# Optimization experiments

Measured on AMD Instinct MI355X. Metric: run time of the kernel, lower is better.

## Reference

```python
import jax, jax.numpy as jnp
import numpy as np

B, N, K = 8, 2048, 100  # graphs per batch, nodes per graph, diffpool clusters


def _bn(x, g, b, eps=1e-5):
    # BatchNorm1d in training mode over all B*N nodes (biased variance)
    m = x.mean(axis=(0, 1))
    v = x.var(axis=(0, 1))
    return (x - m) * jax.lax.rsqrt(v + eps) * g + b


def _norm_adj(A):
    # PyG gcn_norm: add remaining self-loops (fill=1), D^-1/2 (A+I) D^-1/2
    n = A.shape[-1]
    d = jnp.diagonal(A, axis1=-2, axis2=-1)
    A_hat = A + jnp.where(d == 0, 1.0, 0.0)[..., :, None] * jnp.eye(n, dtype=A.dtype)
    deg = A_hat.sum(-1)
    dinv = jnp.where(deg > 0, 1.0 / jnp.sqrt(deg), 0.0)
    return dinv[..., :, None] * A_hat * dinv[..., None, :]


def _gcn(An, x, W, b):
    # GCNConv: propagate(x @ W) + bias, with pre-normalized adjacency
    return An @ (x @ W) + b


def _forward(x, adj, W_in, W3030, Wp13, b30, b100, Wfc_pool, bfc_pool,
             W1, b1, W2, b2, gamma30, beta30, gamma100, beta100):
    A_w = _norm_adj(adj)                               # weighted (edge_attr) adjacency
    A_b = _norm_adj((adj > 0).astype(adj.dtype))       # pool convs ignore edge_attr
    # feature branch
    x11 = _bn(_gcn(A_w, x, W_in[0], b30[0]), gamma30[0], beta30[0])
    x12 = _bn(_gcn(A_w, x11, W3030[0], b30[1]), gamma30[1], beta30[1])
    x13 = _bn(_gcn(A_w, x12, W3030[1], b30[2]), gamma30[2], beta30[2])
    x1_out = jnp.concatenate([x11, x12, x13], -1).max(axis=1)   # [B,90]
    # assignment branch
    s11 = _bn(_gcn(A_b, x, W_in[1], b30[3]), gamma30[3], beta30[3])
    s12 = _bn(_gcn(A_b, s11, W3030[2], b30[4]), gamma30[4], beta30[4])
    s13 = _bn(_gcn(A_b, s12, Wp13, b100), gamma100, beta100)
    s1 = jnp.concatenate([s11, s12, s13], -1) @ Wfc_pool + bfc_pool  # [B,N,K]
    # dense_diff_pool (link/entropy losses are unused by the forward output)
    s = jax.nn.softmax(s1, -1)
    p1_x = jnp.einsum('bnk,bnd->bkd', s, x13)          # s^T x  [B,K,30]
    p1_adj = jnp.einsum('bnk,bnl->bkl', s, adj @ s)    # s^T A s  [B,K,K]
    # second stage on pooled (dense, weighted) graph
    A2 = _norm_adj(p1_adj)
    x21 = _bn(_gcn(A2, p1_x, W3030[3], b30[5]), gamma30[5], beta30[5])
    x22 = _bn(_gcn(A2, x21, W3030[4], b30[6]), gamma30[6], beta30[6])
    x23 = _bn(_gcn(A2, x22, W3030[5], b30[7]), gamma30[7], beta30[7])
    x2_out = jnp.concatenate([x21, x22, x23], -1).max(axis=1)   # [B,90]
    h = jnp.concatenate([x1_out, x2_out], -1) @ W1 + b1
    return jax.nn.relu(h) @ W2 + b2                    # [B,6]


def setup_inputs():
    key = jax.random.key(0)
    ks = jax.random.split(key, 12)
    u = jax.random.uniform(ks[0], (B, N, N), dtype=jnp.float32)
    mask = jax.random.uniform(ks[1], (B, N, N)) < 0.05
    A = jnp.triu(u * mask, 1)
    adj = A + jnp.swapaxes(A, -1, -2)
    x = jax.random.normal(ks[2], (B, N, 3), dtype=jnp.float32)
    w = lambda k, s: jax.random.normal(k, s, dtype=jnp.float32) * 0.1
    return dict(
        x=x, adj=adj,
        W_in=w(ks[3], (2, 3, 30)),      # conv11, pool_conv11
        W3030=w(ks[4], (6, 30, 30)),    # conv12, conv13, pool_conv12, conv21..23
        Wp13=w(ks[5], (30, 100)),
        b30=jnp.zeros((8, 30), jnp.float32),
        b100=jnp.zeros((100,), jnp.float32),
        Wfc_pool=w(ks[6], (160, 100)), bfc_pool=jnp.zeros((100,), jnp.float32),
        W1=w(ks[7], (180, 50)), b1=jnp.zeros((50,), jnp.float32),
        W2=w(ks[8], (50, 6)), b2=jnp.zeros((6,), jnp.float32),
        gamma30=jnp.ones((8, 30), jnp.float32), beta30=jnp.zeros((8, 30), jnp.float32),
        gamma100=jnp.ones((100,), jnp.float32), beta100=jnp.zeros((100,), jnp.float32),
    )


def reference(x, adj, W_in, W3030, Wp13, b30, b100, Wfc_pool, bfc_pool,
              W1, b1, W2, b2, gamma30, beta30, gamma100, beta100):
    return _forward(x, adj, W_in, W3030, Wp13, b30, b100, Wfc_pool, bfc_pool,
                    W1, b1, W2, b2, gamma30, beta30, gamma100, beta100)
```

## Files before the change

kernel.cpp:

```cpp
#include <hip/hip_runtime.h>
#include <hip/hip_fp16.h>
#include <cstdint>
#include <cstddef>

#define BATCH 8
#define NN 2048
#define RTOT 16384

static constexpr size_t OF_B1W   = 0;
static constexpr size_t OF_B1B   = 3840;
static constexpr size_t OF_B2W   = 7680;
static constexpr size_t OF_B2B   = 11520;
static constexpr size_t OF_B3W   = 15360;
static constexpr size_t OF_B3B   = 15840;
static constexpr size_t OF_S2    = 17440;
static constexpr size_t OF_CNT   = 17620;
static constexpr size_t ZEND     = 17632;
static constexpr size_t OF_DINVW = 17664;
static constexpr size_t OF_DINVB = OF_DINVW + 16384;
static constexpr size_t OF_HWBT  = OF_DINVB + 16384;
static constexpr size_t OF_HW3T  = OF_HWBT + 524288;
static constexpr size_t OF_HBT   = OF_HW3T + 262144;
static constexpr size_t OF_ZW    = OF_HBT + 917504;
static constexpr size_t OF_ZB    = OF_ZW + 524288;
static constexpr size_t OF_X11   = OF_ZB + 1703936;
static constexpr size_t OF_X12   = OF_X11 + 524288;
static constexpr size_t OF_X13   = OF_X12 + 524288;
static constexpr size_t OF_S11   = OF_X13 + 524288;
static constexpr size_t OF_S12   = OF_S11 + 524288;
static constexpr size_t OF_PARTMAX = OF_S12 + 524288;
static constexpr size_t OF_PP    = OF_PARTMAX + 23040;
static constexpr size_t OF_PPOOL = OF_PP + 3328000;
static constexpr size_t OF_AW    = OF_PPOOL + 104000;
static constexpr size_t OF_AB    = OF_AW + 16777216;
static constexpr size_t OF_SROW  = OF_AB + 16777216;

typedef _Float16 f16x8 __attribute__((ext_vector_type(8)));
typedef float f32x4 __attribute__((ext_vector_type(4)));

#define FMA4(acc, s, h) { acc.x += (s)*(h).x; acc.y += (s)*(h).y; acc.z += (s)*(h).z; acc.w += (s)*(h).w; }

__device__ __forceinline__ unsigned short f2h(float f) {
  _Float16 h = (_Float16)f;
  return *(unsigned short*)&h;
}
__device__ __forceinline__ float h2f(unsigned short s) {
  _Float16 h = *(_Float16*)&s;
  return (float)h;
}

__device__ __forceinline__ size_t fidx(size_t blk, int lc, int k) {
  return ((blk * 64 + (k >> 5)) * 64 + ((k >> 3) & 3) * 16 + lc) * 8 + (k & 7);
}


__global__ __launch_bounds__(256) void k_build(
    const float* __restrict__ adj, const float* __restrict__ x,
    const float* __restrict__ Win,
    _Float16* __restrict__ Aw, _Float16* __restrict__ Ab,
    float* __restrict__ dinvw, float* __restrict__ dinvb,
    _Float16* __restrict__ HT, float* __restrict__ zbase)
{
  __shared__ float tile[16*516];
  __shared__ float dshw[16], dshb[16];
  int t = threadIdx.x;
  int blk = blockIdx.x;
  int r0 = blk << 4;
  size_t gph = (size_t)(r0 >> 11);
  if (blk < 69) {
    int zi = blk * 256 + t;
    if (zi < (int)ZEND) zbase[zi] = 0.f;
  }
  int lr = t >> 4, ls = t & 15;
  const float* rowp = adj + (size_t)(r0 + lr) * NN;
  float sum = 0.f; int cnt = 0;
  for (int ch = 0; ch < 4; ++ch) {
    int c0 = ch << 9;
    __syncthreads();
    const float4* rp = (const float4*)(rowp + c0);
#pragma unroll
    for (int i = 0; i < 8; ++i) {
      float4 v = rp[ls + (i << 4)];
      sum += v.x + v.y + v.z + v.w;
      cnt += (v.x != 0.f) + (v.y != 0.f) + (v.z != 0.f) + (v.w != 0.f);
      *(float4*)&tile[lr*516 + ls*4 + (i << 6)] = v;
    }
    __syncthreads();
    int kbG = (ch << 4) + lr;
    size_t base = (((size_t)blk * 4096) + (size_t)kbG * 64 + (size_t)ls * 4) * 8;
#pragma unroll
    for (int j = 0; j < 4; ++j) {
      int u = ls*4 + j;
      int kg = u >> 4, lc = u & 15;
      int crel = lr*32 + kg*8;
      const float* src = &tile[lc*516 + crel];
      int R = r0 + lc;
      int cg0 = c0 + crel;
      f16x8 wv, bv;
#pragma unroll
      for (int e = 0; e < 8; ++e) {
        float v = src[e];
        bool dg = (cg0 + e) == R;
        wv[e] = (_Float16)(dg ? 1.f : v);
        bv[e] = (_Float16)((dg || v != 0.f) ? 1.f : 0.f);
      }
      *(f16x8*)(Aw + base + j*8) = wv;
      *(f16x8*)(Ab + base + j*8) = bv;
    }
  }
#pragma unroll
  for (int o = 8; o; o >>= 1) { sum += __shfl_down(sum, o); cnt += __shfl_down(cnt, o); }
  if (ls == 0) {
    int R = r0 + lr;
    float dw = rsqrtf(sum + 1.f), db = rsqrtf((float)cnt + 1.f);
    dinvw[R] = dw; dinvb[R] = db;
    dshw[lr] = dw; dshb[lr] = db;
  }
  __syncthreads();
  {
    int R = r0 + lr, rloc = R & (NN-1);
    float x0 = x[R*3], x1 = x[R*3+1], x2 = x[R*3+2];
#pragma unroll
    for (int e = 0; e < 4; ++e) {
      int c = ls*4 + e;
      int side = c >> 5, cc = c & 31;
      float v = 0.f;
      if (cc < 30) {
        const float* W = Win + side*90;
        v = (x0*W[cc] + x1*W[30+cc] + x2*W[60+cc]) * (side ? dshb[lr] : dshw[lr]);
      }
      HT[fidx(gph*4 + (c >> 4), c & 15, rloc)] = (_Float16)v;
    }
  }
}

__global__ __launch_bounds__(256, 3) void k_gemm_pair(
    const _Float16* __restrict__ Aw, const _Float16* __restrict__ Ab,
    const _Float16* __restrict__ HT,
    const float* __restrict__ dinvw, const float* __restrict__ dinvb,
    float* __restrict__ Zw, float* __restrict__ Zb,
    float* __restrict__ bktW, float* __restrict__ bktB)
{
  __shared__ float zs[32][32];
  int t = threadIdx.x;
  int side = blockIdx.x >> 9;
  int rg = blockIdx.x & 511;
  int row0 = rg << 5;
  size_t g = (size_t)(row0 >> 11);
  int w = t >> 6, l = t & 63, lc = l & 15, kg = l >> 4;
  int rowhalf = w & 1, colhalf = w >> 1;
  const _Float16* A = side ? Ab : Aw;
  size_t rowblk = g*128 + ((row0 & 2047) >> 4) + rowhalf;
  const _Float16* Af = A  + (rowblk * 64) * 512 + l * 8;
  const _Float16* Bf = HT + (((size_t)(g*4 + side*2 + colhalf)) * 64) * 512 + l * 8;
  f32x4 acc = {0,0,0,0};
#pragma unroll 16
  for (int kb = 0; kb < 64; ++kb) {
    f16x8 af = *(const f16x8*)(Af + kb*512);
    f16x8 bf = *(const f16x8*)(Bf + kb*512);
    acc = __builtin_amdgcn_mfma_f32_16x16x32_f16(af, bf, acc, 0, 0, 0);
  }
#pragma unroll
  for (int i = 0; i < 4; ++i) zs[rowhalf*16 + kg*4 + i][colhalf*16 + lc] = acc[i];
  __syncthreads();
  {
    int r = t >> 3, c4 = (t & 7) << 2;
    float d = (side ? dinvb : dinvw)[row0 + r];
    float4 o;
    o.x = zs[r][c4+0] * d; o.y = zs[r][c4+1] * d;
    o.z = zs[r][c4+2] * d; o.w = zs[r][c4+3] * d;
    zs[r][c4+0] = o.x; zs[r][c4+1] = o.y; zs[r][c4+2] = o.z; zs[r][c4+3] = o.w;
    float* Zp = (side ? Zb : Zw) + (((size_t)(row0 + r)) << 5) + c4;
    *(float4*)Zp = o;
  }
  __syncthreads();
  int copy = blockIdx.x & 63;
  if (t < 30) {
    float s1 = 0.f, s2 = 0.f;
    for (int r = 0; r < 32; ++r) { float v = zs[r][t]; s1 += v; s2 += v*v; }
    float* bkt = side ? bktB : bktW;
    atomicAdd(&bkt[(t*64+copy)*2],   s1);
    atomicAdd(&bkt[(t*64+copy)*2+1], s2);
  }
}

__global__ __launch_bounds__(256, 3) void k_gemm_l3(
    const _Float16* __restrict__ Aw, const _Float16* __restrict__ Ab,
    const _Float16* __restrict__ Hw3T, const _Float16* __restrict__ HbT,
    const float* __restrict__ dinvw, const float* __restrict__ dinvb,
    float* __restrict__ Zw, float* __restrict__ Zb,
    float* __restrict__ bktW3, float* __restrict__ bktB3)
{
  __shared__ float zsst[1024];
  int t = threadIdx.x;
  int w = t >> 6, l = t & 63, lc = l & 15, kg = l >> 4;
  if (blockIdx.x < 512) {
    int row0 = blockIdx.x << 5;
    size_t g = (size_t)(row0 >> 11);
    int rowhalf = w & 1, colhalf = w >> 1;
    size_t rowblk = g*128 + ((row0 & 2047) >> 4) + rowhalf;
    const _Float16* Af = Aw   + (rowblk * 64) * 512 + l * 8;
    const _Float16* Bf = Hw3T + (((size_t)(g*2 + colhalf)) * 64) * 512 + l * 8;
    f32x4 acc = {0,0,0,0};
#pragma unroll 16
    for (int kb = 0; kb < 64; ++kb) {
      f16x8 af = *(const f16x8*)(Af + kb*512);
      f16x8 bf = *(const f16x8*)(Bf + kb*512);
      acc = __builtin_amdgcn_mfma_f32_16x16x32_f16(af, bf, acc, 0, 0, 0);
    }
    float (*zs)[32] = (float (*)[32])zsst;
#pragma unroll
    for (int i = 0; i < 4; ++i) zs[rowhalf*16 + kg*4 + i][colhalf*16 + lc] = acc[i];
    __syncthreads();
    {
      int r = t >> 3, c4 = (t & 7) << 2;
      float d = dinvw[row0 + r];
      float4 o;
      o.x = zs[r][c4+0] * d; o.y = zs[r][c4+1] * d;
      o.z = zs[r][c4+2] * d; o.w = zs[r][c4+3] * d;
      zs[r][c4+0] = o.x; zs[r][c4+1] = o.y; zs[r][c4+2] = o.z; zs[r][c4+3] = o.w;
      float* Zp = Zw + (((size_t)(row0 + r)) << 5) + c4;
      *(float4*)Zp = o;
    }
    __syncthreads();
    if (t < 30) {
      float s1 = 0.f, s2 = 0.f;
      for (int r = 0; r < 32; ++r) { float v = zs[r][t]; s1 += v; s2 += v*v; }
      int copy = blockIdx.x & 7;
      atomicAdd(&bktW3[(t*8+copy)*2],   s1);
      atomicAdd(&bktW3[(t*8+copy)*2+1], s2);
    }
  } else {
    int bid = blockIdx.x - 512;
    int row0 = bid << 5;
    size_t g = (size_t)(row0 >> 11);
    int rowhalf = w & 1, fgrp = w >> 1;
    size_t rowblk = g*128 + ((row0 & 2047) >> 4) + rowhalf;
    const _Float16* Af = Ab + (rowblk * 64) * 512 + l * 8;
    for (int s = t; s < 200; s += 256) zsst[s] = 0.f;
    int f0 = fgrp * 4, nf = fgrp ? 3 : 4;
    const _Float16* Bf = HbT + (((size_t)(g*7 + f0)) * 64) * 512 + l * 8;
    f32x4 acc[4];
#pragma unroll
    for (int f = 0; f < 4; ++f) acc[f] = (f32x4){0,0,0,0};
    if (nf == 4) {
#pragma unroll 8
      for (int kb = 0; kb < 64; ++kb) {
        f16x8 af = *(const f16x8*)(Af + kb*512);
#pragma unroll
        for (int f = 0; f < 4; ++f) {
          f16x8 bf = *(const f16x8*)(Bf + (size_t)f*32768 + kb*512);
          acc[f] = __builtin_amdgcn_mfma_f32_16x16x32_f16(af, bf, acc[f], 0, 0, 0);
        }
      }
    } else {
#pragma unroll 8
      for (int kb = 0; kb < 64; ++kb) {
        f16x8 af = *(const f16x8*)(Af + kb*512);
#pragma unroll
        for (int f = 0; f < 3; ++f) {
          f16x8 bf = *(const f16x8*)(Bf + (size_t)f*32768 + kb*512);
          acc[f] = __builtin_amdgcn_mfma_f32_16x16x32_f16(af, bf, acc[f], 0, 0, 0);
        }
      }
    }
    __syncthreads();
    float d[4];
#pragma unroll
    for (int i = 0; i < 4; ++i) d[i] = dinvb[row0 + rowhalf*16 + kg*4 + i];
    for (int f = 0; f < nf; ++f) {
      int col = (f0 + f)*16 + lc;
#pragma unroll
      for (int i = 0; i < 4; ++i) {
        float v = acc[f][i] * d[i];
        int row = row0 + rowhalf*16 + kg*4 + i;
        if (col < 104) Zb[(size_t)row * 104 + col] = v;
        if (col < 100) { atomicAdd(&zsst[col*2], v); atomicAdd(&zsst[col*2+1], v*v); }
      }
    }
    __syncthreads();
    int copy = bid & 7;
    for (int i2 = t; i2 < 200; i2 += 256)
      atomicAdd(&bktB3[((i2>>1)*8 + copy)*2 + (i2&1)], zsst[i2]);
  }
}

__global__ __launch_bounds__(256, 3) void k_gemm_as(
    const _Float16* __restrict__ Aw, const _Float16* __restrict__ ST,
    const unsigned short* __restrict__ Srow, float* __restrict__ As)
{
  int t = threadIdx.x;
  int w = t >> 6, l = t & 63, lc = l & 15, kg = l >> 4;
  int row0 = blockIdx.x << 5;
  size_t g = (size_t)(row0 >> 11);
  int rowhalf = w & 1, fgrp = w >> 1;
  size_t rowblk = g*128 + ((row0 & 2047) >> 4) + rowhalf;
  const _Float16* Af = Aw + (rowblk * 64) * 512 + l * 8;
  int f0 = fgrp * 4, nf = fgrp ? 3 : 4;
  const _Float16* Bf = ST + (((size_t)(g*7 + f0)) * 64) * 512 + l * 8;
  f32x4 acc[4];
#pragma unroll
  for (int f = 0; f < 4; ++f) acc[f] = (f32x4){0,0,0,0};
  if (nf == 4) {
#pragma unroll 8
    for (int kb = 0; kb < 64; ++kb) {
      f16x8 af = *(const f16x8*)(Af + kb*512);
#pragma unroll
      for (int f = 0; f < 4; ++f) {
        f16x8 bf = *(const f16x8*)(Bf + (size_t)f*32768 + kb*512);
        acc[f] = __builtin_amdgcn_mfma_f32_16x16x32_f16(af, bf, acc[f], 0, 0, 0);
      }
    }
  } else {
#pragma unroll 8
    for (int kb = 0; kb < 64; ++kb) {
      f16x8 af = *(const f16x8*)(Af + kb*512);
#pragma unroll
      for (int f = 0; f < 3; ++f) {
        f16x8 bf = *(const f16x8*)(Bf + (size_t)f*32768 + kb*512);
        acc[f] = __builtin_amdgcn_mfma_f32_16x16x32_f16(af, bf, acc[f], 0, 0, 0);
      }
    }
  }
  for (int f = 0; f < nf; ++f) {
    int col = (f0 + f)*16 + lc;
#pragma unroll
    for (int i = 0; i < 4; ++i) {
      int row = row0 + rowhalf*16 + kg*4 + i;
      if (col < 104)
        As[(size_t)row * 104 + col] = acc[f][i] - h2f(Srow[(size_t)row * 104 + col]);
    }
  }
}

template<int LEVEL>
__global__ __launch_bounds__(256) void k_apply_gemm(
    const float* __restrict__ Zw, const float* __restrict__ bktW,
    const float* __restrict__ gW, const float* __restrict__ beW,
    float* __restrict__ xst, const float* __restrict__ Ww,
    const float* __restrict__ dinvw,
    const float* __restrict__ Zb, const float* __restrict__ bktB,
    const float* __restrict__ gB, const float* __restrict__ beB,
    float* __restrict__ sst, const float* __restrict__ Wb,
    const float* __restrict__ dinvb,
    _Float16* __restrict__ HwOutT, _Float16* __restrict__ HbOutT)
{
  constexpr int NGB = (LEVEL == 1) ? 8 : 26;
  constexpr int OSTRIDEB = (LEVEL == 1) ? 32 : 104;
  constexpr int NG = 8 + NGB;
  __shared__ float WwL[30*32];
  __shared__ float WbL[30*OSTRIDEB];
  __shared__ float awL[60], abL[60];
  int t = threadIdx.x;
  if (t < 60) {
    int c = t % 30;
    bool isW = t < 30;
    const float4* p = (const float4*)((isW ? bktW : bktB) + c*128);
    float s1 = 0.f, s2 = 0.f;
#pragma unroll
    for (int k = 0; k < 32; ++k) { float4 v = p[k]; s1 += v.x + v.z; s2 += v.y + v.w; }
    float mean = s1/16384.f, var = s2/16384.f - mean*mean, inv = rsqrtf(var + 1e-5f);
    float aa = (isW ? gW : gB)[c]*inv;
    float* dst = isW ? awL : abL;
    dst[c] = aa; dst[30+c] = (isW ? beW : beB)[c] - mean*aa;
  }
  for (int idx = t; idx < 30*32; idx += 256) {
    int k = idx >> 5, c = idx & 31;
    WwL[idx] = (c < 30) ? Ww[k*30 + c] : 0.f;
  }
  if (LEVEL == 1) {
    for (int idx = t; idx < 30*32; idx += 256) {
      int k = idx >> 5, c = idx & 31;
      WbL[idx] = (c < 30) ? Wb[k*30 + c] : 0.f;
    }
  } else {
    for (int idx = t; idx < 30*OSTRIDEB; idx += 256) {
      int k = idx / OSTRIDEB, j = idx % OSTRIDEB;
      WbL[idx] = (j < 100) ? Wb[k*100 + j] : 0.f;
    }
  }
  __syncthreads();
  int gid = blockIdx.x * 256 + t;
  int row = gid / NG, g = gid % NG;
  size_t gph = (size_t)(row >> 11);
  int rloc = row & (NN-1);
  if (g < 8) {
    const float4* Z4 = (const float4*)Zw + (size_t)row*8;
    float4 z4[8];
#pragma unroll
    for (int u = 0; u < 8; ++u) z4[u] = Z4[u];
    const float* z = (const float*)z4;
    int ch = 4*g;
    float4 zg = Z4[g];
    float4 xv;
    xv.x = (ch+0 < 30) ? awL[ch+0]*zg.x + awL[30+ch+0] : 0.f;
    xv.y = (ch+1 < 30) ? awL[ch+1]*zg.y + awL[30+ch+1] : 0.f;
    xv.z = (ch+2 < 30) ? awL[ch+2]*zg.z + awL[30+ch+2] : 0.f;
    xv.w = (ch+3 < 30) ? awL[ch+3]*zg.w + awL[30+ch+3] : 0.f;
    ((float4*)xst)[(size_t)row*8+g] = xv;
    float4 o = {0,0,0,0};
#pragma unroll
    for (int k = 0; k < 30; ++k) {
      float xk = awL[k]*z[k] + awL[30+k];
      float4 w = *(const float4*)(WwL + k*32 + 4*g);
      FMA4(o, xk, w);
    }
    float d = dinvw[row];
    float ov[4] = {d*o.x, d*o.y, d*o.z, d*o.w};
#pragma unroll
    for (int i = 0; i < 4; ++i) {
      int col = ch + i;
      if (LEVEL == 1) HwOutT[fidx(gph*4 + (col>>4), col & 15, rloc)] = (_Float16)ov[i];
      else            HwOutT[fidx(gph*2 + (col>>4), col & 15, rloc)] = (_Float16)ov[i];
    }
  } else {
    int gb = g - 8;
    const float4* Z4 = (const float4*)Zb + (size_t)row*8;
    float4 z4[8];
#pragma unroll
    for (int u = 0; u < 8; ++u) z4[u] = Z4[u];
    const float* z = (const float*)z4;
    if (gb < 8) {
      int ch = 4*gb;
      float4 zg = Z4[gb];
      float4 sv;
      sv.x = (ch+0 < 30) ? abL[ch+0]*zg.x + abL[30+ch+0] : 0.f;
      sv.y = (ch+1 < 30) ? abL[ch+1]*zg.y + abL[30+ch+1] : 0.f;
      sv.z = (ch+2 < 30) ? abL[ch+2]*zg.z + abL[30+ch+2] : 0.f;
      sv.w = (ch+3 < 30) ? abL[ch+3]*zg.w + abL[30+ch+3] : 0.f;
      ((float4*)sst)[(size_t)row*8+gb] = sv;
    }
    float4 o = {0,0,0,0};
#pragma unroll
    for (int k = 0; k < 30; ++k) {
      float sk = abL[k]*z[k] + abL[30+k];
      float4 w = *(const float4*)(WbL + k*OSTRIDEB + 4*gb);
      FMA4(o, sk, w);
    }
    float d = dinvb[row];
    float ov[4] = {d*o.x, d*o.y, d*o.z, d*o.w};
#pragma unroll
    for (int i = 0; i < 4; ++i) {
      int col = 4*gb + i;
      if (LEVEL == 1) { int c2 = 32 + col; HbOutT[fidx(gph*4 + (c2>>4), c2 & 15, rloc)] = (_Float16)ov[i]; }
      else            HbOutT[fidx(gph*7 + (col>>4), col & 15, rloc)] = (_Float16)ov[i];
    }
    if (LEVEL == 2) {
      if (gb == 24) {
#pragma unroll
        for (int c = 104; c < 108; ++c) HbOutT[fidx(gph*7 + 6, c & 15, rloc)] = (_Float16)0.f;
      } else if (gb == 25) {
#pragma unroll
        for (int c = 108; c < 112; ++c) HbOutT[fidx(gph*7 + 6, c & 15, rloc)] = (_Float16)0.f;
      }
    }
  }
}

__global__ __launch_bounds__(256) void k_fcpool(
    const float* __restrict__ Zw3, const float* __restrict__ bktW3,
    const float* __restrict__ gW3, const float* __restrict__ beW3,
    const float* __restrict__ Zb3, const float* __restrict__ bktB3,
    const float* __restrict__ g100, const float* __restrict__ be100,
    const float* __restrict__ s11, const float* __restrict__ s12,
    const float* __restrict__ Wfc, const float* __restrict__ bfc,
    float* __restrict__ x13, unsigned short* __restrict__ Srow,
    _Float16* __restrict__ ST)
{
  __shared__ float shm[14240];
  __shared__ float aw3[60], ab3[200];
  float* feat = shm;
  float* Wl = shm + 10240;
  int t = threadIdx.x;
  int g0 = blockIdx.x * 64;
  size_t gph = (size_t)(g0 >> 11);
  if (t < 30) {
    const float4* p = (const float4*)(bktW3 + t*16);
    float s1 = 0.f, s2 = 0.f;
#pragma unroll
    for (int k = 0; k < 4; ++k) { float4 v = p[k]; s1 += v.x + v.z; s2 += v.y + v.w; }
    float mean = s1/16384.f, var = s2/16384.f - mean*mean, inv = rsqrtf(var + 1e-5f);
    float aa = gW3[t]*inv; aw3[t] = aa; aw3[30+t] = beW3[t] - mean*aa;
  } else if (t >= 64 && t < 164) {
    int c = t - 64;
    const float4* p = (const float4*)(bktB3 + c*16);
    float s1 = 0.f, s2 = 0.f;
#pragma unroll
    for (int k = 0; k < 4; ++k) { float4 v = p[k]; s1 += v.x + v.z; s2 += v.y + v.w; }
    float mean = s1/16384.f, var = s2/16384.f - mean*mean, inv = rsqrtf(var + 1e-5f);
    float aa = g100[c]*inv; ab3[c] = aa; ab3[100+c] = be100[c] - mean*aa;
  }
  __syncthreads();
  for (int idx = t; idx < 64*160; idx += 256) {
    int l = idx / 160, c = idx % 160;
    int g = g0 + l;
    float v;
    if (c < 30) v = s11[(size_t)g*32 + c];
    else if (c < 60) v = s12[(size_t)g*32 + (c-30)];
    else { int k = c - 60; v = ab3[k]*Zb3[(size_t)g*104 + k] + ab3[100 + k]; }
    feat[l*160 + c] = v;
  }
  for (int idx = t; idx < 64*32; idx += 256) {
    int l = idx >> 5, c = idx & 31;
    int g = g0 + l;
    x13[(size_t)g*32+c] = (c < 30) ? aw3[c]*Zw3[(size_t)g*32+c] + aw3[30+c] : 0.f;
  }
  int np = t >> 3, kg = t & 7;
  int n0 = np*2, n1 = np*2 + 1;
  int kbase = kg*12 + (kg < 4 ? kg : 4);
  int klen  = kg < 4 ? 13 : 12;
  float a0[13], a1[13];
#pragma unroll
  for (int j = 0; j < 13; ++j) { a0[j] = 0.f; a1[j] = 0.f; }
  for (int ch = 0; ch < 4; ++ch) {
    __syncthreads();
    for (int idx = t; idx < 4000; idx += 256) {
      int r = idx/100, j = idx%100;
      Wl[r*100 + j] = Wfc[(ch*40 + r)*100 + j];
    }
    __syncthreads();
    for (int kk = 0; kk < 40; ++kk) {
      float f0 = feat[n0*160 + ch*40+kk];
      float f1 = feat[n1*160 + ch*40+kk];
#pragma unroll
      for (int j = 0; j < 13; ++j) {
        if (j < klen) {
          float w = Wl[kk*100 + kbase + j];
          a0[j] += f0*w; a1[j] += f1*w;
        }
      }
    }
  }
  __syncthreads();
  float* sRow = shm;
  for (int j = 0; j < klen; ++j) {
    int k = kbase + j;
    sRow[n0*100 + k] = a0[j] + bfc[k];
    sRow[n1*100 + k] = a1[j] + bfc[k];
  }
  __syncthreads();
  int n = t >> 2, part = t & 3;
  int i0 = part*25;
  int rloc = (g0 + n) & (NN-1);
  float m = -3.4e38f;
  for (int i = 0; i < 25; ++i) m = fmaxf(m, sRow[n*100 + i0 + i]);
  m = fmaxf(m, __shfl_xor(m, 1));
  m = fmaxf(m, __shfl_xor(m, 2));
  float ev[25]; float s = 0.f;
  for (int i = 0; i < 25; ++i) { float e = __expf(sRow[n*100 + i0 + i] - m); ev[i] = e; s += e; }
  s += __shfl_xor(s, 1);
  s += __shfl_xor(s, 2);
  float rinv = 1.f / s;
  for (int i = 0; i < 25; ++i) {
    float v = ev[i] * rinv;
    int c = i0 + i;
    Srow[(size_t)(g0+n)*104 + c] = f2h(v);
    ST[fidx(gph*7 + (c>>4), c & 15, rloc)] = (_Float16)v;
  }
  if (part == 3) {
#pragma unroll
    for (int c = 100; c < 104; ++c) Srow[(size_t)(g0+n)*104 + c] = 0;
#pragma unroll
    for (int c = 100; c < 112; ++c) ST[fidx(gph*7 + (c>>4), c & 15, rloc)] = (_Float16)0.f;
  }
}

__global__ __launch_bounds__(256) void k_pool_part(
    const unsigned short* __restrict__ S, const float* __restrict__ x13,
    const float* __restrict__ As, const float* __restrict__ x11,
    const float* __restrict__ x12, float* __restrict__ pp, float* __restrict__ pm)
{
  __shared__ float sL[64][100];
  __shared__ float xL[64][132];
  __shared__ float red[256];
  int t = threadIdx.x;
  int b = blockIdx.x >> 5, chunk = blockIdx.x & 31;
  int g0 = b * 2048 + chunk * 64;
  int kt = t/10, dt = t%10;
  int k0 = kt*4, d0 = dt*13;
  float acc[4][13];
#pragma unroll
  for (int a = 0; a < 4; ++a)
#pragma unroll
    for (int j = 0; j < 13; ++j) acc[a][j] = 0.f;
  for (int idx = t; idx < 64*100; idx += 256) {
    int l = idx/100, k = idx%100;
    sL[l][k] = h2f(S[(size_t)(g0+l)*104 + k]);
  }
  for (int idx = t; idx < 64*130; idx += 256) {
    int l = idx/130, d = idx%130;
    xL[l][d] = d < 30 ? x13[(size_t)(g0+l)*32 + d] : As[(size_t)(g0+l)*104 + (d-30)];
  }
  __syncthreads();
  if (t < 250) {
    for (int kk = 0; kk < 64; ++kk) {
      float sv[4];
#pragma unroll
      for (int a = 0; a < 4; ++a) sv[a] = sL[kk][k0+a];
#pragma unroll
      for (int j = 0; j < 13; ++j) {
        float xv = xL[kk][d0+j];
#pragma unroll
        for (int a = 0; a < 4; ++a) acc[a][j] += sv[a]*xv;
      }
    }
    float* dst = pp + (size_t)blockIdx.x * 13000;
    for (int a = 0; a < 4; ++a)
      for (int j = 0; j < 13; ++j)
        dst[(k0+a)*130 + (d0+j)] = acc[a][j];
  }
  __syncthreads();
  {
    int c = t & 31, rg = t >> 5;
    const float* srcs[3] = {x11, x12, x13};
#pragma unroll
    for (int a = 0; a < 3; ++a) {
      const float* p = srcs[a] + (size_t)(g0+rg)*32 + c;
      float m = -3.4e38f;
#pragma unroll
      for (int it = 0; it < 8; ++it) m = fmaxf(m, p[it*256]);
      red[t] = m;
      __syncthreads();
      if (t < 30) {
        float mm = red[t];
        for (int g = 1; g < 8; ++g) mm = fmaxf(mm, red[g*32+t]);
        pm[(size_t)blockIdx.x*90 + a*30 + t] = mm;
      }
      __syncthreads();
    }
  }
}

__global__ __launch_bounds__(256) void k_pool_reduce(
    const float* __restrict__ pp, float* __restrict__ ppool)
{
  int b = blockIdx.x / 51, blk = blockIdx.x % 51;
  int idx = blk * 256 + threadIdx.x;
  if (idx < 13000) {
    const float* src = pp + (size_t)b * 32 * 13000 + idx;
    float s = 0.f;
#pragma unroll
    for (int c = 0; c < 32; ++c) s += src[c*13000];
    ppool[(size_t)b*13000 + idx] = s;
  }
}

__global__ __launch_bounds__(256) void k_s2fused(
    const float* __restrict__ ppool, const float* __restrict__ partmax,
    const float* __restrict__ Wm,
    const float* __restrict__ g30,
    const float* __restrict__ be30,
    float* __restrict__ bktS2,
    int* __restrict__ cnt,
    const float* __restrict__ W1, const float* __restrict__ b1,
    const float* __restrict__ W2, const float* __restrict__ b2,
    float* __restrict__ out)
{
  __shared__ float A2f[10000];
  __shared__ float buf1[3000];
  __shared__ float buf2[3200];
  __shared__ float WL[960];
  __shared__ float dl[100];
  __shared__ float st1[30], st2[30];
  __shared__ float coef[60];
  __shared__ float x1L[90], x2L[90], hh[50];
  int b = blockIdx.x, t = threadIdx.x;
  for (int idx = t; idx < 13000; idx += 256) {
    float s = ppool[(size_t)b*13000 + idx];
    int k = idx/130, d = idx%130;
    if (d < 30) buf1[k*30 + d] = s;
    else A2f[k*100 + (d-30)] = s;
  }
  __syncthreads();
  if (t < 100 && A2f[t*101] == 0.f) A2f[t*101] = 1.f;
  __syncthreads();
  if (t < 100) {
    float s = 0.f;
    for (int j = 0; j < 100; ++j) s += A2f[t*100 + j];
    dl[t] = s > 0.f ? rsqrtf(s) : 0.f;
  }
  __syncthreads();
  for (int idx = t; idx < 10000; idx += 256) {
    int i = idx/100, j = idx%100;
    A2f[idx] = dl[i]*dl[j]*A2f[idx];
  }
  int rp = t >> 2, cg = t & 3;
  int i0 = rp*2, c0 = cg*8;
  bool act = (t < 200);
  for (int L = 0; L < 3; ++L) {
    if (t < 30) { st1[t] = 0.f; st2[t] = 0.f; }
    const float* W = Wm + L*900;
    for (int idx = t; idx < 960; idx += 256) {
      int k = idx >> 5, c = idx & 31;
      WL[idx] = (c < 30) ? W[k*30 + c] : 0.f;
    }
    __syncthreads();
    if (act) {
      float a0[8] = {0,0,0,0,0,0,0,0}, a1[8] = {0,0,0,0,0,0,0,0};
      for (int k = 0; k < 30; ++k) {
        float xx0 = buf1[i0*30 + k], xx1 = buf1[(i0+1)*30 + k];
        float4 w0 = *(const float4*)&WL[k*32 + c0];
        float4 w1 = *(const float4*)&WL[k*32 + c0 + 4];
        a0[0] += xx0*w0.x; a0[1] += xx0*w0.y; a0[2] += xx0*w0.z; a0[3] += xx0*w0.w;
        a0[4] += xx0*w1.x; a0[5] += xx0*w1.y; a0[6] += xx0*w1.z; a0[7] += xx0*w1.w;
        a1[0] += xx1*w0.x; a1[1] += xx1*w0.y; a1[2] += xx1*w0.z; a1[3] += xx1*w0.w;
        a1[4] += xx1*w1.x; a1[5] += xx1*w1.y; a1[6] += xx1*w1.z; a1[7] += xx1*w1.w;
      }
      float4 s00 = {a0[0],a0[1],a0[2],a0[3]}, s01 = {a0[4],a0[5],a0[6],a0[7]};
      float4 s10 = {a1[0],a1[1],a1[2],a1[3]}, s11v = {a1[4],a1[5],a1[6],a1[7]};
      *(float4*)&buf2[i0*32 + c0]       = s00;
      *(float4*)&buf2[i0*32 + c0 + 4]   = s01;
      *(float4*)&buf2[(i0+1)*32 + c0]   = s10;
      *(float4*)&buf2[(i0+1)*32 + c0+4] = s11v;
    }
    __syncthreads();
    if (act) {
      float z0[8] = {0,0,0,0,0,0,0,0}, z1[8] = {0,0,0,0,0,0,0,0};
      for (int j = 0; j < 100; ++j) {
        float av0 = A2f[i0*100 + j], av1 = A2f[(i0+1)*100 + j];
        float4 t0 = *(const float4*)&buf2[j*32 + c0];
        float4 t1 = *(const float4*)&buf2[j*32 + c0 + 4];
        z0[0] += av0*t0.x; z0[1] += av0*t0.y; z0[2] += av0*t0.z; z0[3] += av0*t0.w;
        z0[4] += av0*t1.x; z0[5] += av0*t1.y; z0[6] += av0*t1.z; z0[7] += av0*t1.w;
        z1[0] += av1*t0.x; z1[1] += av1*t0.y; z1[2] += av1*t0.z; z1[3] += av1*t0.w;
        z1[4] += av1*t1.x; z1[5] += av1*t1.y; z1[6] += av1*t1.z; z1[7] += av1*t1.w;
      }
#pragma unroll
      for (int k = 0; k < 8; ++k) {
        int c = c0 + k;
        if (c < 30) {
          buf1[i0*30 + c]     = z0[k];
          buf1[(i0+1)*30 + c] = z1[k];
          atomicAdd(&st1[c], z0[k] + z1[k]);
          atomicAdd(&st2[c], z0[k]*z0[k] + z1[k]*z1[k]);
        }
      }
    }
    __syncthreads();
    if (t < 30) {
      atomicAdd(&bktS2[(L*30+t)*2],   st1[t]);
      atomicAdd(&bktS2[(L*30+t)*2+1], st2[t]);
    }
    __syncthreads();
    if (t == 0) {
      __threadfence();
      atomicAdd(cnt, 1);
      while (atomicAdd(cnt, 0) < (L+1)*8) {}
      __threadfence();
    }
    __syncthreads();
    if (t < 30) {
      float s1 = atomicAdd(&bktS2[(L*30+t)*2],   0.f);
      float s2 = atomicAdd(&bktS2[(L*30+t)*2+1], 0.f);
      float mean = s1/800.f, var = s2/800.f - mean*mean, inv = rsqrtf(var + 1e-5f);
      float aa = g30[L*30+t]*inv;
      coef[t] = aa; coef[30+t] = be30[L*30+t] - mean*aa;
    }
    __syncthreads();
    if (L < 2) {
      for (int idx = t; idx < 3000; idx += 256) {
        int c = idx % 30;
        buf1[idx] = coef[c]*buf1[idx] + coef[30+c];
      }
      __syncthreads();
      if (t < 30) {
        float m = -3.4e38f;
        for (int i = 0; i < 100; ++i) m = fmaxf(m, buf1[i*30+t]);
        x2L[L*30+t] = m;
      }
      __syncthreads();
    } else {
      if (t < 30) {
        float m = -3.4e38f;
        for (int i = 0; i < 100; ++i) m = fmaxf(m, coef[t]*buf1[i*30+t] + coef[30+t]);
        x2L[60+t] = m;
      }
    }
  }
  if (t < 90) {
    float m = -3.4e38f;
    for (int s = 0; s < 32; ++s) m = fmaxf(m, partmax[(size_t)(b*32+s)*90 + t]);
    x1L[t] = m;
  }
  __syncthreads();
  if (t < 50) {
    float a = b1[t];
    for (int k = 0; k < 90; ++k) a += x1L[k]*W1[k*50+t];
    for (int k = 0; k < 90; ++k) a += x2L[k]*W1[(90+k)*50+t];
    hh[t] = fmaxf(a, 0.f);
  }
  __syncthreads();
  if (t < 6) {
    float a = b2[t];
    for (int j = 0; j < 50; ++j) a += hh[j]*W2[j*6+t];
    out[b*6+t] = a;
  }
}

extern "C" void kernel_launch(void* const* d_in, const int* in_sizes, int n_in,
                              void* d_out, int out_size, void* d_ws, size_t ws_size,
                              hipStream_t stream)
{
  const float* x    = (const float*)d_in[0];
  const float* adj  = (const float*)d_in[1];
  const float* Win  = (const float*)d_in[2];
  const float* W3030= (const float*)d_in[3];
  const float* Wp13 = (const float*)d_in[4];
  const float* Wfc  = (const float*)d_in[7];
  const float* bfc  = (const float*)d_in[8];
  const float* W1   = (const float*)d_in[9];
  const float* b1   = (const float*)d_in[10];
  const float* W2   = (const float*)d_in[11];
  const float* b2   = (const float*)d_in[12];
  const float* g30  = (const float*)d_in[13];
  const float* be30 = (const float*)d_in[14];
  const float* g100 = (const float*)d_in[15];
  const float* be100= (const float*)d_in[16];
  float* out = (float*)d_out;

  float* wsf = (float*)d_ws;
  float* bL1W = wsf + OF_B1W;  float* bL1B = wsf + OF_B1B;
  float* bL2W = wsf + OF_B2W;  float* bL2B = wsf + OF_B2B;
  float* bL3W = wsf + OF_B3W;  float* bL3B = wsf + OF_B3B;
  float* bktS2 = wsf + OF_S2;
  int*   cnt  = (int*)(wsf + OF_CNT);
  float* dinvw = wsf + OF_DINVW;
  float* dinvb = wsf + OF_DINVB;
  _Float16* HwbT = (_Float16*)(wsf + OF_HWBT);
  _Float16* Hw3T = (_Float16*)(wsf + OF_HW3T);
  _Float16* HbT  = (_Float16*)(wsf + OF_HBT);
  float* Zw = wsf + OF_ZW;
  float* Zb = wsf + OF_ZB;
  float* x11 = wsf + OF_X11;
  float* x12 = wsf + OF_X12;
  float* x13 = wsf + OF_X13;
  float* s11 = wsf + OF_S11;
  float* s12 = wsf + OF_S12;
  float* pp  = wsf + OF_PP;
  float* ppool = wsf + OF_PPOOL;
  float* partmax = wsf + OF_PARTMAX;
  _Float16* Aw = (_Float16*)(wsf + OF_AW);
  _Float16* Ab = (_Float16*)(wsf + OF_AB);
  unsigned short* Srow = (unsigned short*)(wsf + OF_SROW);

  k_build<<<1024, 256, 0, stream>>>(adj, x, Win, Aw, Ab, dinvw, dinvb, HwbT, wsf);

  k_gemm_pair<<<1024, 256, 0, stream>>>(Aw, Ab, HwbT, dinvw, dinvb, Zw, Zb, bL1W, bL1B);
  k_apply_gemm<1><<<1024, 256, 0, stream>>>(Zw, bL1W, g30+0, be30+0, x11, W3030+0, dinvw,
                                            Zb, bL1B, g30+90, be30+90, s11, W3030+2*900, dinvb, HwbT, HwbT);

  k_gemm_pair<<<1024, 256, 0, stream>>>(Aw, Ab, HwbT, dinvw, dinvb, Zw, Zb, bL2W, bL2B);
  k_apply_gemm<2><<<2176, 256, 0, stream>>>(Zw, bL2W, g30+30, be30+30, x12, W3030+900, dinvw,
                                            Zb, bL2B, g30+120, be30+120, s12, Wp13, dinvb, Hw3T, HbT);

  k_gemm_l3<<<1024, 256, 0, stream>>>(Aw, Ab, Hw3T, HbT, dinvw, dinvb, Zw, Zb, bL3W, bL3B);
  k_fcpool<<<256, 256, 0, stream>>>(Zw, bL3W, g30+60, be30+60, Zb, bL3B, g100, be100,
                                    s11, s12, Wfc, bfc, x13, Srow, HbT );

  k_gemm_as<<<512, 256, 0, stream>>>(Aw, HbT , Srow, Zb );
  k_pool_part<<<256, 256, 0, stream>>>(Srow, x13, Zb, x11, x12, pp, partmax);
  k_pool_reduce<<<408, 256, 0, stream>>>(pp, ppool);

  k_s2fused<<<BATCH, 256, 0, stream>>>(ppool, partmax, W3030+3*900, g30+150, be30+150,
                                       bktS2, cnt, W1, b1, W2, b2, out);
}
```

Baseline: 641.5 us.

## Derive binary adjacency on the fly from weighted fp16 adjacency tiles

Stops materializing the separate fp16 binary adjacency. Instead, each GEMM kernel loads the weighted adjacency tile once and builds the 0/1 mask in registers. The weighted and binary propagation GEMMs are fused into one block per row group, halving adjacency reads and removing a 32MB write in the build kernel. This adds per-element compare work in the inner loop and changes the warp split in the layer-3 kernel. It relies on the diagonal being stored as 1 in the weighted tile, so it stays nonzero in the mask.

```diff
diff --git a/kernel.cpp b/kernel.cpp
--- a/kernel.cpp
+++ b/kernel.cpp
@@ -32,8 +32,7 @@
 static constexpr size_t OF_PP    = OF_PARTMAX + 23040;
 static constexpr size_t OF_PPOOL = OF_PP + 3328000;
 static constexpr size_t OF_AW    = OF_PPOOL + 104000;
-static constexpr size_t OF_AB    = OF_AW + 16777216;
-static constexpr size_t OF_SROW  = OF_AB + 16777216;
+static constexpr size_t OF_SROW  = OF_AW + 16777216;
 
 typedef _Float16 f16x8 __attribute__((ext_vector_type(8)));
 typedef float f32x4 __attribute__((ext_vector_type(4)));
@@ -49,6 +48,13 @@
   return (float)h;
 }
 
+__device__ __forceinline__ f16x8 binz(f16x8 a) {
+  f16x8 r;
+#pragma unroll
+  for (int e = 0; e < 8; ++e) r[e] = (a[e] != (_Float16)0.f) ? (_Float16)1.f : (_Float16)0.f;
+  return r;
+}
+
 __device__ __forceinline__ size_t fidx(size_t blk, int lc, int k) {
   return ((blk * 64 + (k >> 5)) * 64 + ((k >> 3) & 3) * 16 + lc) * 8 + (k & 7);
 }
@@ -57,7 +63,7 @@
 __global__ __launch_bounds__(256) void k_build(
     const float* __restrict__ adj, const float* __restrict__ x,
     const float* __restrict__ Win,
-    _Float16* __restrict__ Aw, _Float16* __restrict__ Ab,
+    _Float16* __restrict__ Aw,
     float* __restrict__ dinvw, float* __restrict__ dinvb,
     _Float16* __restrict__ HT, float* __restrict__ zbase)
 {
@@ -96,16 +102,14 @@
       const float* src = &tile[lc*516 + crel];
       int R = r0 + lc;
       int cg0 = c0 + crel;
-      f16x8 wv, bv;
+      f16x8 wv;
 #pragma unroll
       for (int e = 0; e < 8; ++e) {
         float v = src[e];
         bool dg = (cg0 + e) == R;
         wv[e] = (_Float16)(dg ? 1.f : v);
-        bv[e] = (_Float16)((dg || v != 0.f) ? 1.f : 0.f);
       }
       *(f16x8*)(Aw + base + j*8) = wv;
-      *(f16x8*)(Ab + base + j*8) = bv;
     }
   }
 #pragma unroll
@@ -135,154 +139,159 @@
 }
 
 __global__ __launch_bounds__(256, 3) void k_gemm_pair(
-    const _Float16* __restrict__ Aw, const _Float16* __restrict__ Ab,
-    const _Float16* __restrict__ HT,
+    const _Float16* __restrict__ Aw, const _Float16* __restrict__ HT,
     const float* __restrict__ dinvw, const float* __restrict__ dinvb,
     float* __restrict__ Zw, float* __restrict__ Zb,
     float* __restrict__ bktW, float* __restrict__ bktB)
 {
-  __shared__ float zs[32][32];
+  __shared__ float zsW[32][32];
+  __shared__ float zsB[32][32];
   int t = threadIdx.x;
-  int side = blockIdx.x >> 9;
-  int rg = blockIdx.x & 511;
-  int row0 = rg << 5;
+  int row0 = blockIdx.x << 5;
   size_t g = (size_t)(row0 >> 11);
   int w = t >> 6, l = t & 63, lc = l & 15, kg = l >> 4;
   int rowhalf = w & 1, colhalf = w >> 1;
-  const _Float16* A = side ? Ab : Aw;
   size_t rowblk = g*128 + ((row0 & 2047) >> 4) + rowhalf;
-  const _Float16* Af = A  + (rowblk * 64) * 512 + l * 8;
-  const _Float16* Bf = HT + (((size_t)(g*4 + side*2 + colhalf)) * 64) * 512 + l * 8;
-  f32x4 acc = {0,0,0,0};
-#pragma unroll 16
+  const _Float16* Af  = Aw + (rowblk * 64) * 512 + l * 8;
+  const _Float16* BfW = HT + (((size_t)(g*4 + colhalf)) * 64) * 512 + l * 8;
+  const _Float16* BfB = HT + (((size_t)(g*4 + 2 + colhalf)) * 64) * 512 + l * 8;
+  f32x4 accW = {0,0,0,0}, accB = {0,0,0,0};
+#pragma unroll 8
   for (int kb = 0; kb < 64; ++kb) {
-    f16x8 af = *(const f16x8*)(Af + kb*512);
-    f16x8 bf = *(const f16x8*)(Bf + kb*512);
-    acc = __builtin_amdgcn_mfma_f32_16x16x32_f16(af, bf, acc, 0, 0, 0);
-  }
-#pragma unroll
-  for (int i = 0; i < 4; ++i) zs[rowhalf*16 + kg*4 + i][colhalf*16 + lc] = acc[i];
+    f16x8 af = *(const f16x8*)(Af  + kb*512);
+    f16x8 bw = *(const f16x8*)(BfW + kb*512);
+    f16x8 bb = *(const f16x8*)(BfB + kb*512);
+    f16x8 ab = binz(af);
+    accW = __builtin_amdgcn_mfma_f32_16x16x32_f16(af, bw, accW, 0, 0, 0);
+    accB = __builtin_amdgcn_mfma_f32_16x16x32_f16(ab, bb, accB, 0, 0, 0);
+  }
+#pragma unroll
+  for (int i = 0; i < 4; ++i) {
+    zsW[rowhalf*16 + kg*4 + i][colhalf*16 + lc] = accW[i];
+    zsB[rowhalf*16 + kg*4 + i][colhalf*16 + lc] = accB[i];
+  }
   __syncthreads();
   {
     int r = t >> 3, c4 = (t & 7) << 2;
-    float d = (side ? dinvb : dinvw)[row0 + r];
-    float4 o;
-    o.x = zs[r][c4+0] * d; o.y = zs[r][c4+1] * d;
-    o.z = zs[r][c4+2] * d; o.w = zs[r][c4+3] * d;
-    zs[r][c4+0] = o.x; zs[r][c4+1] = o.y; zs[r][c4+2] = o.z; zs[r][c4+3] = o.w;
-    float* Zp = (side ? Zb : Zw) + (((size_t)(row0 + r)) << 5) + c4;
-    *(float4*)Zp = o;
+    float dW = dinvw[row0 + r], dB = dinvb[row0 + r];
+    float4 oW, oB;
+    oW.x = zsW[r][c4+0]*dW; oW.y = zsW[r][c4+1]*dW;
+    oW.z = zsW[r][c4+2]*dW; oW.w = zsW[r][c4+3]*dW;
+    oB.x = zsB[r][c4+0]*dB; oB.y = zsB[r][c4+1]*dB;
+    oB.z = zsB[r][c4+2]*dB; oB.w = zsB[r][c4+3]*dB;
+    zsW[r][c4+0]=oW.x; zsW[r][c4+1]=oW.y; zsW[r][c4+2]=oW.z; zsW[r][c4+3]=oW.w;
+    zsB[r][c4+0]=oB.x; zsB[r][c4+1]=oB.y; zsB[r][c4+2]=oB.z; zsB[r][c4+3]=oB.w;
+    *(float4*)(Zw + (((size_t)(row0 + r)) << 5) + c4) = oW;
+    *(float4*)(Zb + (((size_t)(row0 + r)) << 5) + c4) = oB;
   }
   __syncthreads();
   int copy = blockIdx.x & 63;
   if (t < 30) {
     float s1 = 0.f, s2 = 0.f;
-    for (int r = 0; r < 32; ++r) { float v = zs[r][t]; s1 += v; s2 += v*v; }
-    float* bkt = side ? bktB : bktW;
-    atomicAdd(&bkt[(t*64+copy)*2],   s1);
-    atomicAdd(&bkt[(t*64+copy)*2+1], s2);
+    for (int r = 0; r < 32; ++r) { float v = zsW[r][t]; s1 += v; s2 += v*v; }
+    atomicAdd(&bktW[(t*64+copy)*2],   s1);
+    atomicAdd(&bktW[(t*64+copy)*2+1], s2);
+  } else if (t >= 64 && t < 94) {
+    int c = t - 64;
+    float s1 = 0.f, s2 = 0.f;
+    for (int r = 0; r < 32; ++r) { float v = zsB[r][c]; s1 += v; s2 += v*v; }
+    atomicAdd(&bktB[(c*64+copy)*2],   s1);
+    atomicAdd(&bktB[(c*64+copy)*2+1], s2);
   }
 }
 
 __global__ __launch_bounds__(256, 3) void k_gemm_l3(
-    const _Float16* __restrict__ Aw, const _Float16* __restrict__ Ab,
+    const _Float16* __restrict__ Aw,
     const _Float16* __restrict__ Hw3T, const _Float16* __restrict__ HbT,
     const float* __restrict__ dinvw, const float* __restrict__ dinvb,
     float* __restrict__ Zw, float* __restrict__ Zb,
     float* __restrict__ bktW3, float* __restrict__ bktB3)
 {
-  __shared__ float zsst[1024];
+  __shared__ float zsW[32][32];
+  __shared__ float st[200];
   int t = threadIdx.x;
   int w = t >> 6, l = t & 63, lc = l & 15, kg = l >> 4;
-  if (blockIdx.x < 512) {
-    int row0 = blockIdx.x << 5;
-    size_t g = (size_t)(row0 >> 11);
-    int rowhalf = w & 1, colhalf = w >> 1;
-    size_t rowblk = g*128 + ((row0 & 2047) >> 4) + rowhalf;
-    const _Float16* Af = Aw   + (rowblk * 64) * 512 + l * 8;
-    const _Float16* Bf = Hw3T + (((size_t)(g*2 + colhalf)) * 64) * 512 + l * 8;
-    f32x4 acc = {0,0,0,0};
-#pragma unroll 16
+  int rowhalf = w & 1, grp = w >> 1;
+  int row0 = blockIdx.x << 5;
+  size_t g = (size_t)(row0 >> 11);
+  size_t rowblk = g*128 + ((row0 & 2047) >> 4) + rowhalf;
+  const _Float16* Af = Aw + (rowblk * 64) * 512 + l * 8;
+  for (int s = t; s < 200; s += 256) st[s] = 0.f;
+  f32x4 accW0 = {0,0,0,0}, accW1 = {0,0,0,0};
+  f32x4 accB[4];
+#pragma unroll
+  for (int f = 0; f < 4; ++f) accB[f] = (f32x4){0,0,0,0};
+  if (grp == 0) {
+    const _Float16* Bw0 = Hw3T + (((size_t)(g*2)) * 64) * 512 + l * 8;
+    const _Float16* Bw1 = Bw0 + (size_t)64 * 512;
+    const _Float16* Bb  = HbT + (((size_t)(g*7)) * 64) * 512 + l * 8;
+#pragma unroll 4
     for (int kb = 0; kb < 64; ++kb) {
       f16x8 af = *(const f16x8*)(Af + kb*512);
-      f16x8 bf = *(const f16x8*)(Bf + kb*512);
-      acc = __builtin_amdgcn_mfma_f32_16x16x32_f16(af, bf, acc, 0, 0, 0);
-    }
-    float (*zs)[32] = (float (*)[32])zsst;
-#pragma unroll
-    for (int i = 0; i < 4; ++i) zs[rowhalf*16 + kg*4 + i][colhalf*16 + lc] = acc[i];
-    __syncthreads();
-    {
-      int r = t >> 3, c4 = (t & 7) << 2;
-      float d = dinvw[row0 + r];
-      float4 o;
-      o.x = zs[r][c4+0] * d; o.y = zs[r][c4+1] * d;
-      o.z = zs[r][c4+2] * d; o.w = zs[r][c4+3] * d;
-      zs[r][c4+0] = o.x; zs[r][c4+1] = o.y; zs[r][c4+2] = o.z; zs[r][c4+3] = o.w;
-      float* Zp = Zw + (((size_t)(row0 + r)) << 5) + c4;
-      *(float4*)Zp = o;
-    }
-    __syncthreads();
-    if (t < 30) {
-      float s1 = 0.f, s2 = 0.f;
-      for (int r = 0; r < 32; ++r) { float v = zs[r][t]; s1 += v; s2 += v*v; }
-      int copy = blockIdx.x & 7;
-      atomicAdd(&bktW3[(t*8+copy)*2],   s1);
-      atomicAdd(&bktW3[(t*8+copy)*2+1], s2);
+      f16x8 ab = binz(af);
+      accW0 = __builtin_amdgcn_mfma_f32_16x16x32_f16(af, *(const f16x8*)(Bw0 + kb*512), accW0, 0, 0, 0);
+      accW1 = __builtin_amdgcn_mfma_f32_16x16x32_f16(af, *(const f16x8*)(Bw1 + kb*512), accW1, 0, 0, 0);
+      accB[0] = __builtin_amdgcn_mfma_f32_16x16x32_f16(ab, *(const f16x8*)(Bb +           kb*512), accB[0], 0, 0, 0);
+      accB[1] = __builtin_amdgcn_mfma_f32_16x16x32_f16(ab, *(const f16x8*)(Bb + 32768  + kb*512), accB[1], 0, 0, 0);
+      accB[2] = __builtin_amdgcn_mfma_f32_16x16x32_f16(ab, *(const f16x8*)(Bb + 65536  + kb*512), accB[2], 0, 0, 0);
     }
   } else {
-    int bid = blockIdx.x - 512;
-    int row0 = bid << 5;
-    size_t g = (size_t)(row0 >> 11);
-    int rowhalf = w & 1, fgrp = w >> 1;
-    size_t rowblk = g*128 + ((row0 & 2047) >> 4) + rowhalf;
-    const _Float16* Af = Ab + (rowblk * 64) * 512 + l * 8;
-    for (int s = t; s < 200; s += 256) zsst[s] = 0.f;
-    int f0 = fgrp * 4, nf = fgrp ? 3 : 4;
-    const _Float16* Bf = HbT + (((size_t)(g*7 + f0)) * 64) * 512 + l * 8;
-    f32x4 acc[4];
-#pragma unroll
-    for (int f = 0; f < 4; ++f) acc[f] = (f32x4){0,0,0,0};
-    if (nf == 4) {
-#pragma unroll 8
-      for (int kb = 0; kb < 64; ++kb) {
-        f16x8 af = *(const f16x8*)(Af + kb*512);
-#pragma unroll
-        for (int f = 0; f < 4; ++f) {
-          f16x8 bf = *(const f16x8*)(Bf + (size_t)f*32768 + kb*512);
-          acc[f] = __builtin_amdgcn_mfma_f32_16x16x32_f16(af, bf, acc[f], 0, 0, 0);
-        }
-      }
-    } else {
-#pragma unroll 8
-      for (int kb = 0; kb < 64; ++kb) {
-        f16x8 af = *(const f16x8*)(Af + kb*512);
-#pragma unroll
-        for (int f = 0; f < 3; ++f) {
-          f16x8 bf = *(const f16x8*)(Bf + (size_t)f*32768 + kb*512);
-          acc[f] = __builtin_amdgcn_mfma_f32_16x16x32_f16(af, bf, acc[f], 0, 0, 0);
-        }
-      }
-    }
-    __syncthreads();
+    const _Float16* Bb = HbT + (((size_t)(g*7 + 3)) * 64) * 512 + l * 8;
+#pragma unroll 4
+    for (int kb = 0; kb < 64; ++kb) {
+      f16x8 af = *(const f16x8*)(Af + kb*512);
+      f16x8 ab = binz(af);
+#pragma unroll
+      for (int f = 0; f < 4; ++f) {
+        f16x8 bf = *(const f16x8*)(Bb + (size_t)f*32768 + kb*512);
+        accB[f] = __builtin_amdgcn_mfma_f32_16x16x32_f16(ab, bf, accB[f], 0, 0, 0);
+      }
+    }
+  }
+  if (grp == 0) {
+#pragma unroll
+    for (int i = 0; i < 4; ++i) {
+      zsW[rowhalf*16 + kg*4 + i][lc]      = accW0[i];
+      zsW[rowhalf*16 + kg*4 + i][16 + lc] = accW1[i];
+    }
+  }
+  __syncthreads();
+  {
+    int r = t >> 3, c4 = (t & 7) << 2;
+    float d = dinvw[row0 + r];
+    float4 o;
+    o.x = zsW[r][c4+0]*d; o.y = zsW[r][c4+1]*d;
+    o.z = zsW[r][c4+2]*d; o.w = zsW[r][c4+3]*d;
+    zsW[r][c4+0]=o.x; zsW[r][c4+1]=o.y; zsW[r][c4+2]=o.z; zsW[r][c4+3]=o.w;
+    *(float4*)(Zw + (((size_t)(row0 + r)) << 5) + c4) = o;
+  }
+  {
     float d[4];
 #pragma unroll
     for (int i = 0; i < 4; ++i) d[i] = dinvb[row0 + rowhalf*16 + kg*4 + i];
+    int fbase = grp ? 3 : 0;
+    int nf = grp ? 4 : 3;
     for (int f = 0; f < nf; ++f) {
-      int col = (f0 + f)*16 + lc;
+      int col = (fbase + f)*16 + lc;
 #pragma unroll
       for (int i = 0; i < 4; ++i) {
-        float v = acc[f][i] * d[i];
+        float v = accB[f][i] * d[i];
         int row = row0 + rowhalf*16 + kg*4 + i;
         if (col < 104) Zb[(size_t)row * 104 + col] = v;
-        if (col < 100) { atomicAdd(&zsst[col*2], v); atomicAdd(&zsst[col*2+1], v*v); }
-      }
-    }
-    __syncthreads();
-    int copy = bid & 7;
-    for (int i2 = t; i2 < 200; i2 += 256)
-      atomicAdd(&bktB3[((i2>>1)*8 + copy)*2 + (i2&1)], zsst[i2]);
-  }
+        if (col < 100) { atomicAdd(&st[col*2], v); atomicAdd(&st[col*2+1], v*v); }
+      }
+    }
+  }
+  __syncthreads();
+  int copy = blockIdx.x & 7;
+  if (t < 30) {
+    float s1 = 0.f, s2 = 0.f;
+    for (int r = 0; r < 32; ++r) { float v = zsW[r][t]; s1 += v; s2 += v*v; }
+    atomicAdd(&bktW3[(t*8+copy)*2],   s1);
+    atomicAdd(&bktW3[(t*8+copy)*2+1], s2);
+  }
+  for (int i2 = t; i2 < 200; i2 += 256)
+    atomicAdd(&bktB3[((i2>>1)*8 + copy)*2 + (i2&1)], st[i2]);
 }
 
 __global__ __launch_bounds__(256, 3) void k_gemm_as(
@@ -840,20 +849,19 @@
   float* ppool = wsf + OF_PPOOL;
   float* partmax = wsf + OF_PARTMAX;
   _Float16* Aw = (_Float16*)(wsf + OF_AW);
-  _Float16* Ab = (_Float16*)(wsf + OF_AB);
   unsigned short* Srow = (unsigned short*)(wsf + OF_SROW);
 
-  k_build<<<1024, 256, 0, stream>>>(adj, x, Win, Aw, Ab, dinvw, dinvb, HwbT, wsf);
-
-  k_gemm_pair<<<1024, 256, 0, stream>>>(Aw, Ab, HwbT, dinvw, dinvb, Zw, Zb, bL1W, bL1B);
+  k_build<<<1024, 256, 0, stream>>>(adj, x, Win, Aw, dinvw, dinvb, HwbT, wsf);
+
+  k_gemm_pair<<<512, 256, 0, stream>>>(Aw, HwbT, dinvw, dinvb, Zw, Zb, bL1W, bL1B);
   k_apply_gemm<1><<<1024, 256, 0, stream>>>(Zw, bL1W, g30+0, be30+0, x11, W3030+0, dinvw,
                                             Zb, bL1B, g30+90, be30+90, s11, W3030+2*900, dinvb, HwbT, HwbT);
 
-  k_gemm_pair<<<1024, 256, 0, stream>>>(Aw, Ab, HwbT, dinvw, dinvb, Zw, Zb, bL2W, bL2B);
+  k_gemm_pair<<<512, 256, 0, stream>>>(Aw, HwbT, dinvw, dinvb, Zw, Zb, bL2W, bL2B);
   k_apply_gemm<2><<<2176, 256, 0, stream>>>(Zw, bL2W, g30+30, be30+30, x12, W3030+900, dinvw,
                                             Zb, bL2B, g30+120, be30+120, s12, Wp13, dinvb, Hw3T, HbT);
 
-  k_gemm_l3<<<1024, 256, 0, stream>>>(Aw, Ab, Hw3T, HbT, dinvw, dinvb, Zw, Zb, bL3W, bL3B);
+  k_gemm_l3<<<512, 256, 0, stream>>>(Aw, Hw3T, HbT, dinvw, dinvb, Zw, Zb, bL3W, bL3B);
   k_fcpool<<<256, 256, 0, stream>>>(Zw, bL3W, g30+60, be30+60, Zb, bL3B, g100, be100,
                                     s11, s12, Wfc, bfc, x13, Srow, HbT );
 
```

New measurement: 593.4 us. 7.5% less time.
